# Performance work log

Hardware: AMD Instinct MI355X
Metric: run time of the kernel (lower is better)

Reference implementation:

```python
import jax, jax.numpy as jnp
import numpy as np

ALPHA = 0.2  # LeakyReLU negative slope
NEG_BIG = -9e15

def setup_inputs() -> dict:
    key = jax.random.key(0)
    k1, k2, k3, k4 = jax.random.split(key, 4)
    B, N, Fin, Fout = 32, 1024, 64, 64
    x = jax.random.normal(k1, (B, N, Fin), dtype=jnp.float32)
    adj = jax.random.randint(k2, (B, N, N), 0, 2, dtype=jnp.int32)
    W = jax.random.normal(k3, (Fin, Fout), dtype=jnp.float32) * (1.414 / np.sqrt(Fin))
    a = jax.random.normal(k4, (2 * Fout, 1), dtype=jnp.float32) * 0.1
    return {"x": x, "adj": adj, "W": W, "a": a}

def reference(x, adj, W, a):
    # x: [B,N,Fin], adj: [B,N,N], W: [Fin,Fout], a: [2*Fout,1]
    h = jnp.einsum('bnf,fo->bno', x, W)               # [B,N,Fout]
    Fout = W.shape[1]
    a1 = a[:Fout, 0]                                   # source half
    a2 = a[Fout:, 0]                                   # target half
    # e_ij = leakyrelu(a1.h_i + a2.h_j)  (equivalent to concat+matmul)
    f = h @ a1                                         # [B,N]
    g = h @ a2                                         # [B,N]
    e = jax.nn.leaky_relu(f[:, :, None] + g[:, None, :], ALPHA)  # [B,N,N]
    att = jnp.where(adj > 0, e, jnp.float32(NEG_BIG))
    att = jax.nn.softmax(att, axis=2)                  # dropout p=0, eval mode
    h_prime = jnp.einsum('bij,bjo->bio', att, h)       # [B,N,Fout]
    return jax.nn.elu(h_prime)                         # concat=True -> elu
```

## Files before the change

kernel.cpp:

```cpp
#include <hip/hip_runtime.h>
#include <hip/hip_bf16.h>
#include <hip/hip_fp16.h>

#define NN 1024
#define FD 64
#define BB 32

typedef __attribute__((ext_vector_type(4))) float    f32x4;
typedef __attribute__((ext_vector_type(8))) _Float16 f16x8;

static __device__ __forceinline__ unsigned short f2hu(float x) {
  _Float16 h = (_Float16)x;
  return __builtin_bit_cast(unsigned short, h);
}
static __device__ __forceinline__ f16x8 bch(int4 v) {
  return __builtin_bit_cast(f16x8, v);
}

__global__ __launch_bounds__(256) void gat_k1(
    const float* __restrict__ x, const float* __restrict__ W,
    const float* __restrict__ av, float* __restrict__ fv,
    float* __restrict__ gv, unsigned short* __restrict__ hF)
{
  __shared__ __align__(16) float Wl[FD * FD];
  __shared__ __align__(16) float xl[FD * 68];
  __shared__ __align__(16) unsigned short tl[FD * 64];
  __shared__ __align__(16) float al[2 * FD];

  const int tid = threadIdx.x;
  const int b   = blockIdx.x >> 4;
  const int n0  = (blockIdx.x & 15) << 6;

  if (tid < 32) ((f32x4*)al)[tid] = ((const f32x4*)av)[tid];
  {
    const int r  = tid >> 2;
    const int cb = (tid & 3) << 2;
    const f32x4* Wg = (const f32x4*)W;
    const f32x4* xg = (const f32x4*)(x + ((size_t)(b * NN + n0)) * FD);
#pragma unroll
    for (int k = 0; k < 4; ++k) {
      f32x4 wv = Wg[r * 16 + cb + k];
      f32x4 xv = xg[r * 16 + cb + k];
      *(f32x4*)(Wl + r * FD + ((cb + k) << 2)) = wv;
      *(f32x4*)(xl + r * 68 + ((cb + k) << 2)) = xv;
    }
  }
  __syncthreads();

  const int r  = tid >> 2;
  const int o0 = (tid & 3) << 4;
  float acc[16];
#pragma unroll
  for (int i = 0; i < 16; ++i) acc[i] = 0.f;

#pragma unroll 8
  for (int f = 0; f < FD; ++f) {
    float xv = xl[r * 68 + f];
    const f32x4* wr = (const f32x4*)(Wl + f * FD + o0);
#pragma unroll
    for (int c = 0; c < 4; ++c) {
      f32x4 wv = wr[c];
      acc[c * 4 + 0] += xv * wv.x;
      acc[c * 4 + 1] += xv * wv.y;
      acc[c * 4 + 2] += xv * wv.z;
      acc[c * 4 + 3] += xv * wv.w;
    }
  }

  float fp = 0.f, gp = 0.f;
#pragma unroll
  for (int i = 0; i < 16; ++i) {
    fp += acc[i] * al[o0 + i];
    gp += acc[i] * al[FD + o0 + i];
  }
  fp += __shfl_xor(fp, 1); fp += __shfl_xor(fp, 2);
  gp += __shfl_xor(gp, 1); gp += __shfl_xor(gp, 2);
  if ((tid & 3) == 0) {
    fv[b * NN + n0 + r] = fp;
    gv[b * NN + n0 + r] = gp;
  }

#pragma unroll
  for (int i = 0; i < 16; ++i) {
    int o = o0 + i;
    tl[o * 64 + ((((r >> 3) ^ (o & 7)) << 3) | (r & 7))] = f2hu(acc[i]);
  }
  __syncthreads();

  {
    const int jt = n0 >> 6;
#pragma unroll
    for (int hh = 0; hh < 2; ++hh) {
      int u = tid + (hh << 8);
      int frag = u >> 6, l = u & 63;
      int o = ((frag >> 1) << 4) + (l & 15);
      int c = ((frag & 1) << 2) + (l >> 4);
      int4 v = *(const int4*)(tl + o * 64 + ((c ^ (o & 7)) << 3));
      *(int4*)(hF + ((((size_t)(b * 16 + jt)) * 8 + frag) * 64 + l) * 8) = v;
    }
  }
}

__global__ __launch_bounds__(256) void gat_k2(
    const int* __restrict__ adj, const float* __restrict__ fv,
    const float* __restrict__ gv, const unsigned short* __restrict__ hF,
    float* __restrict__ out)
{
  __shared__ __align__(16) float gl[NN];
  __shared__ float red[4];

  const int tid  = threadIdx.x;
  const int b    = blockIdx.x >> 4;
  const int i0   = (blockIdx.x & 15) << 6;
  const int lane = tid & 63, w = tid >> 6;
  const int m16  = lane & 15, hi = lane >> 4;
  const int bN   = b * NN;

  f32x4 g4 = *(const f32x4*)(gv + bN + tid * 4);
  *(f32x4*)(gl + tid * 4) = g4;
  float gm = fmaxf(fmaxf(g4.x, g4.y), fmaxf(g4.z, g4.w));
  float fm = fv[bN + i0 + lane];
#pragma unroll
  for (int m = 1; m < 64; m <<= 1) {
    gm = fmaxf(gm, __shfl_xor(gm, m));
    fm = fmaxf(fm, __shfl_xor(fm, m));
  }
  if (lane == 0) red[w] = gm;
  const float fr = fv[bN + i0 + w * 16 + m16];
  __syncthreads();
  gm = fmaxf(fmaxf(red[0], red[1]), fmaxf(red[2], red[3]));
  const float sm = fm + gm;
  const float Cb = fmaxf(sm, 0.2f * sm);

  const int*  adjP = adj + ((size_t)(bN + i0 + w * 16 + m16)) * NN + hi * 8;
  const int4* hFb  = (const int4*)hF + (size_t)b * 8192 + lane;

  float dAcc = 0.f;
  f32x4 acc[4];
#pragma unroll
  for (int n = 0; n < 4; ++n) acc[n] = (f32x4){0.f, 0.f, 0.f, 0.f};

  int4 Aa0, Aa1, Aa2, Aa3, Ba0, Ba1, Ba2, Ba3;

#define LADJ(P, t) do { const int o_ = (t) << 6;        \
    P##0 = *(const int4*)(adjP + o_);                   \
    P##1 = *(const int4*)(adjP + o_ + 4);               \
    P##2 = *(const int4*)(adjP + o_ + 32);              \
    P##3 = *(const int4*)(adjP + o_ + 36); } while (0)

#define PCOMP(dst, ia, ib, ga, gb) do {                                    \
    float e0 = fr + ga.x, e1 = fr + ga.y, e2 = fr + ga.z, e3 = fr + ga.w;  \
    float e4 = fr + gb.x, e5 = fr + gb.y, e6 = fr + gb.z, e7 = fr + gb.w;  \
    e0 = fmaxf(e0, 0.2f * e0) - Cb; e1 = fmaxf(e1, 0.2f * e1) - Cb;        \
    e2 = fmaxf(e2, 0.2f * e2) - Cb; e3 = fmaxf(e3, 0.2f * e3) - Cb;        \
    e4 = fmaxf(e4, 0.2f * e4) - Cb; e5 = fmaxf(e5, 0.2f * e5) - Cb;        \
    e6 = fmaxf(e6, 0.2f * e6) - Cb; e7 = fmaxf(e7, 0.2f * e7) - Cb;        \
    float p0 = (ia.x > 0) ? __expf(e0) : 0.f;                              \
    float p1 = (ia.y > 0) ? __expf(e1) : 0.f;                              \
    float p2 = (ia.z > 0) ? __expf(e2) : 0.f;                              \
    float p3 = (ia.w > 0) ? __expf(e3) : 0.f;                              \
    float p4 = (ib.x > 0) ? __expf(e4) : 0.f;                              \
    float p5 = (ib.y > 0) ? __expf(e5) : 0.f;                              \
    float p6 = (ib.z > 0) ? __expf(e6) : 0.f;                              \
    float p7 = (ib.w > 0) ? __expf(e7) : 0.f;                              \
    dAcc += ((p0 + p1) + (p2 + p3)) + ((p4 + p5) + (p6 + p7));             \
    dst = (f16x8){(_Float16)p0, (_Float16)p1, (_Float16)p2, (_Float16)p3,  \
                  (_Float16)p4, (_Float16)p5, (_Float16)p6, (_Float16)p7}; \
  } while (0)

#define TILE(P, t) do {                                                    \
    const int jb_ = (t) << 6;                                              \
    const int4* hp_ = hFb + (size_t)(t) * 512;                             \
    int4 h0_ = hp_[0],   h1_ = hp_[64],  h2_ = hp_[128], h3_ = hp_[192];   \
    int4 h4_ = hp_[256], h5_ = hp_[320], h6_ = hp_[384], h7_ = hp_[448];   \
    f32x4 ga0_ = *(const f32x4*)(gl + jb_ + hi * 8);                       \
    f32x4 ga1_ = *(const f32x4*)(gl + jb_ + hi * 8 + 4);                   \
    f32x4 gb0_ = *(const f32x4*)(gl + jb_ + 32 + hi * 8);                  \
    f32x4 gb1_ = *(const f32x4*)(gl + jb_ + 32 + hi * 8 + 4);              \
    f16x8 pa_, pb_;                                                        \
    PCOMP(pa_, P##0, P##1, ga0_, ga1_);                                    \
    PCOMP(pb_, P##2, P##3, gb0_, gb1_);                                    \
    acc[0] = __builtin_amdgcn_mfma_f32_16x16x32_f16(pa_, bch(h0_), acc[0], 0, 0, 0); \
    acc[0] = __builtin_amdgcn_mfma_f32_16x16x32_f16(pb_, bch(h1_), acc[0], 0, 0, 0); \
    acc[1] = __builtin_amdgcn_mfma_f32_16x16x32_f16(pa_, bch(h2_), acc[1], 0, 0, 0); \
    acc[1] = __builtin_amdgcn_mfma_f32_16x16x32_f16(pb_, bch(h3_), acc[1], 0, 0, 0); \
    acc[2] = __builtin_amdgcn_mfma_f32_16x16x32_f16(pa_, bch(h4_), acc[2], 0, 0, 0); \
    acc[2] = __builtin_amdgcn_mfma_f32_16x16x32_f16(pb_, bch(h5_), acc[2], 0, 0, 0); \
    acc[3] = __builtin_amdgcn_mfma_f32_16x16x32_f16(pa_, bch(h6_), acc[3], 0, 0, 0); \
    acc[3] = __builtin_amdgcn_mfma_f32_16x16x32_f16(pb_, bch(h7_), acc[3], 0, 0, 0); \
  } while (0)

  LADJ(Aa, 0);
  for (int tt = 0; tt < 8; ++tt) {
    LADJ(Ba, 2 * tt + 1);
    TILE(Aa, 2 * tt);
    if (tt < 7) LADJ(Aa, 2 * tt + 2);
    TILE(Ba, 2 * tt + 1);
  }

  dAcc += __shfl_xor(dAcc, 16);
  dAcc += __shfl_xor(dAcc, 32);

  float* outB = out + ((size_t)(bN + i0 + w * 16)) * FD;
#pragma unroll
  for (int rr = 0; rr < 4; ++rr) {
    const int lr = hi * 4 + rr;
    float d   = __shfl(dAcc, lr);
    float inv = d > 0.f ? 1.f / d : 0.f;
#pragma unroll
    for (int n = 0; n < 4; ++n) {
      float v = acc[n][rr] * inv;
      v = v > 0.f ? v : (__expf(v) - 1.f);
      outB[(size_t)lr * FD + n * 16 + m16] = v;
    }
  }
#undef LADJ
#undef PCOMP
#undef TILE
}

extern "C" void kernel_launch(void* const* d_in, const int* in_sizes, int n_in,
                              void* d_out, int out_size, void* d_ws, size_t ws_size,
                              hipStream_t stream) {
  const float* x   = (const float*)d_in[0];
  const int*   adj = (const int*)d_in[1];
  const float* W   = (const float*)d_in[2];
  const float* a   = (const float*)d_in[3];
  float* out = (float*)d_out;

  unsigned short* hF = (unsigned short*)d_ws;
  float* fv = (float*)((char*)d_ws + (size_t)BB * FD * NN * 2);
  float* gv = fv + (size_t)BB * NN;

  gat_k1<<<dim3(BB * 16), dim3(256), 0, stream>>>(x, W, a, fv, gv, hF);
  gat_k2<<<dim3(BB * 16), dim3(256), 0, stream>>>(adj, fv, gv, hF, out);
}
```

Measured before the change: 44.30 us.

## Pack adjacency into bitmask in first kernel and consume bits in attention kernel

Merges the projection kernel with a new adjacency-packing pass: 4 of every 5 blocks read int32 adj rows and write a per-lane-ordered bitmask, so the attention kernel reads 1 bit per edge instead of 4 bytes. The attention loop is also rewritten to double-buffer the h fragment loads across tiles. The full adj array is still read once in the first kernel, so total traffic barely drops. The gain depends on that read running with better parallelism in the wider grid, and on the second kernel overlapping more compute with its now smaller loads.

```diff
diff --git a/kernel.cpp b/kernel.cpp
--- a/kernel.cpp
+++ b/kernel.cpp
@@ -17,93 +17,135 @@
   return __builtin_bit_cast(f16x8, v);
 }
 
-__global__ __launch_bounds__(256) void gat_k1(
+__global__ __launch_bounds__(256) void gat_k01(
     const float* __restrict__ x, const float* __restrict__ W,
-    const float* __restrict__ av, float* __restrict__ fv,
-    float* __restrict__ gv, unsigned short* __restrict__ hF)
+    const float* __restrict__ av, const int* __restrict__ adj,
+    float* __restrict__ fv, float* __restrict__ gv,
+    unsigned short* __restrict__ hF, unsigned* __restrict__ maskG)
 {
-  __shared__ __align__(16) float Wl[FD * FD];
-  __shared__ __align__(16) float xl[FD * 68];
-  __shared__ __align__(16) unsigned short tl[FD * 64];
-  __shared__ __align__(16) float al[2 * FD];
-
+  __shared__ __align__(16) char smem[43008];
   const int tid = threadIdx.x;
-  const int b   = blockIdx.x >> 4;
-  const int n0  = (blockIdx.x & 15) << 6;
-
-  if (tid < 32) ((f32x4*)al)[tid] = ((const f32x4*)av)[tid];
-  {
+  const int id  = blockIdx.x;
+
+  if (id % 5 == 0) {
+    const int kb = id / 5;
+    float*          Wl = (float*)smem;
+    float*          xl = (float*)(smem + 16384);
+    unsigned short* tl = (unsigned short*)(smem + 33792);
+    float*          al = (float*)(smem + 41984);
+
+    const int b  = kb >> 4;
+    const int n0 = (kb & 15) << 6;
+
+    if (tid < 32) ((f32x4*)al)[tid] = ((const f32x4*)av)[tid];
+    {
+      const int r  = tid >> 2;
+      const int cb = (tid & 3) << 2;
+      const f32x4* Wg = (const f32x4*)W;
+      const f32x4* xg = (const f32x4*)(x + ((size_t)(b * NN + n0)) * FD);
+#pragma unroll
+      for (int k = 0; k < 4; ++k) {
+        f32x4 wv = Wg[r * 16 + cb + k];
+        f32x4 xv = xg[r * 16 + cb + k];
+        *(f32x4*)(Wl + r * FD + ((cb + k) << 2)) = wv;
+        *(f32x4*)(xl + r * 68 + ((cb + k) << 2)) = xv;
+      }
+    }
+    __syncthreads();
+
     const int r  = tid >> 2;
-    const int cb = (tid & 3) << 2;
-    const f32x4* Wg = (const f32x4*)W;
-    const f32x4* xg = (const f32x4*)(x + ((size_t)(b * NN + n0)) * FD);
-#pragma unroll
-    for (int k = 0; k < 4; ++k) {
-      f32x4 wv = Wg[r * 16 + cb + k];
-      f32x4 xv = xg[r * 16 + cb + k];
-      *(f32x4*)(Wl + r * FD + ((cb + k) << 2)) = wv;
-      *(f32x4*)(xl + r * 68 + ((cb + k) << 2)) = xv;
-    }
-  }
-  __syncthreads();
-
-  const int r  = tid >> 2;
-  const int o0 = (tid & 3) << 4;
-  float acc[16];
-#pragma unroll
-  for (int i = 0; i < 16; ++i) acc[i] = 0.f;
+    const int o0 = (tid & 3) << 4;
+    float acc[16];
+#pragma unroll
+    for (int i = 0; i < 16; ++i) acc[i] = 0.f;
 
 #pragma unroll 8
-  for (int f = 0; f < FD; ++f) {
-    float xv = xl[r * 68 + f];
-    const f32x4* wr = (const f32x4*)(Wl + f * FD + o0);
-#pragma unroll
-    for (int c = 0; c < 4; ++c) {
-      f32x4 wv = wr[c];
-      acc[c * 4 + 0] += xv * wv.x;
-      acc[c * 4 + 1] += xv * wv.y;
-      acc[c * 4 + 2] += xv * wv.z;
-      acc[c * 4 + 3] += xv * wv.w;
-    }
-  }
-
-  float fp = 0.f, gp = 0.f;
-#pragma unroll
-  for (int i = 0; i < 16; ++i) {
-    fp += acc[i] * al[o0 + i];
-    gp += acc[i] * al[FD + o0 + i];
-  }
-  fp += __shfl_xor(fp, 1); fp += __shfl_xor(fp, 2);
-  gp += __shfl_xor(gp, 1); gp += __shfl_xor(gp, 2);
-  if ((tid & 3) == 0) {
-    fv[b * NN + n0 + r] = fp;
-    gv[b * NN + n0 + r] = gp;
-  }
-
-#pragma unroll
-  for (int i = 0; i < 16; ++i) {
-    int o = o0 + i;
-    tl[o * 64 + ((((r >> 3) ^ (o & 7)) << 3) | (r & 7))] = f2hu(acc[i]);
-  }
-  __syncthreads();
-
-  {
-    const int jt = n0 >> 6;
-#pragma unroll
-    for (int hh = 0; hh < 2; ++hh) {
-      int u = tid + (hh << 8);
-      int frag = u >> 6, l = u & 63;
-      int o = ((frag >> 1) << 4) + (l & 15);
-      int c = ((frag & 1) << 2) + (l >> 4);
-      int4 v = *(const int4*)(tl + o * 64 + ((c ^ (o & 7)) << 3));
-      *(int4*)(hF + ((((size_t)(b * 16 + jt)) * 8 + frag) * 64 + l) * 8) = v;
+    for (int f = 0; f < FD; ++f) {
+      float xv = xl[r * 68 + f];
+      const f32x4* wr = (const f32x4*)(Wl + f * FD + o0);
+#pragma unroll
+      for (int c = 0; c < 4; ++c) {
+        f32x4 wv = wr[c];
+        acc[c * 4 + 0] += xv * wv.x;
+        acc[c * 4 + 1] += xv * wv.y;
+        acc[c * 4 + 2] += xv * wv.z;
+        acc[c * 4 + 3] += xv * wv.w;
+      }
+    }
+
+    float fp = 0.f, gp = 0.f;
+#pragma unroll
+    for (int i = 0; i < 16; ++i) {
+      fp += acc[i] * al[o0 + i];
+      gp += acc[i] * al[FD + o0 + i];
+    }
+    fp += __shfl_xor(fp, 1); fp += __shfl_xor(fp, 2);
+    gp += __shfl_xor(gp, 1); gp += __shfl_xor(gp, 2);
+    if ((tid & 3) == 0) {
+      fv[b * NN + n0 + r] = fp;
+      gv[b * NN + n0 + r] = gp;
+    }
+
+#pragma unroll
+    for (int i = 0; i < 16; ++i) {
+      int o = o0 + i;
+      tl[o * 64 + ((((r >> 3) ^ (o & 7)) << 3) | (r & 7))] = f2hu(acc[i]);
+    }
+    __syncthreads();
+    {
+      const int jt = n0 >> 6;
+#pragma unroll
+      for (int hh = 0; hh < 2; ++hh) {
+        int u = tid + (hh << 8);
+        int frag = u >> 6, l = u & 63;
+        int o = ((frag >> 1) << 4) + (l & 15);
+        int c = ((frag & 1) << 2) + (l >> 4);
+        int4 v = *(const int4*)(tl + o * 64 + ((c ^ (o & 7)) << 3));
+        *(int4*)(hF + ((((size_t)(b * 16 + jt)) * 8 + frag) * 64 + l) * 8) = v;
+      }
+    }
+  } else {
+    const int c  = id - id / 5 - 1;
+    unsigned* mbuf = (unsigned*)smem;
+    const int b = c >> 6, G = c & 63;
+    const int w = tid >> 6, l = tid & 63;
+    const int rr = l >> 4, col16 = l & 15;
+    const int row = G * 16 + w * 4 + rr;
+    const int4* src = (const int4*)(adj + ((size_t)(b * NN + row)) * NN) + col16;
+
+    int4 v[16];
+#pragma unroll
+    for (int q = 0; q < 16; ++q) v[q] = src[q * 16];
+
+#pragma unroll
+    for (int q = 0; q < 16; ++q) {
+      int4 a = v[q];
+      unsigned nib = (unsigned)a.x | ((unsigned)a.y << 1) |
+                     ((unsigned)a.z << 2) | ((unsigned)a.w << 3);
+      unsigned nb  = nib | ((unsigned)__shfl_xor((int)nib, 1) << 4);
+      if (!(l & 1)) {
+        const int hi   = (l >> 1) & 3;
+        const int half = (l >> 3) & 1;
+        const int lam  = hi * 16 + w * 4 + rr;
+        const int p    = q >> 1;
+        const int bp   = (q & 1) * 2 + half;
+        ((char*)smem)[(lam + p * 64) * 4 + bp] = (char)(nb & 0xff);
+      }
+    }
+    __syncthreads();
+    {
+      const int lam = tid >> 2, p0 = (tid & 3) * 2;
+      unsigned w0 = mbuf[lam + p0 * 64];
+      unsigned w1 = mbuf[lam + p0 * 64 + 64];
+      uint2 o; o.x = w0; o.y = w1;
+      *(uint2*)(maskG + (((size_t)(b * 64 + G) * 64 + lam) * 8 + p0)) = o;
     }
   }
 }
 
 __global__ __launch_bounds__(256) void gat_k2(
-    const int* __restrict__ adj, const float* __restrict__ fv,
-    const float* __restrict__ gv, const unsigned short* __restrict__ hF,
+    const float* __restrict__ fv, const float* __restrict__ gv,
+    const unsigned short* __restrict__ hF, const unsigned* __restrict__ maskG,
     float* __restrict__ out)
 {
   __shared__ __align__(16) float gl[NN];
@@ -132,71 +174,70 @@
   const float sm = fm + gm;
   const float Cb = fmaxf(sm, 0.2f * sm);
 
-  const int*  adjP = adj + ((size_t)(bN + i0 + w * 16 + m16)) * NN + hi * 8;
-  const int4* hFb  = (const int4*)hF + (size_t)b * 8192 + lane;
+  const uint4* mp = (const uint4*)(maskG +
+      ((size_t)(b * 64 + (blockIdx.x & 15) * 4 + w) * 64 + lane) * 8);
+  const uint4 mA = mp[0], mB = mp[1];
+  const unsigned mq[8] = {mA.x, mA.y, mA.z, mA.w, mB.x, mB.y, mB.z, mB.w};
+
+  const int4* hFb = (const int4*)hF + (size_t)b * 8192 + lane;
 
   float dAcc = 0.f;
   f32x4 acc[4];
 #pragma unroll
   for (int n = 0; n < 4; ++n) acc[n] = (f32x4){0.f, 0.f, 0.f, 0.f};
 
-  int4 Aa0, Aa1, Aa2, Aa3, Ba0, Ba1, Ba2, Ba3;
-
-#define LADJ(P, t) do { const int o_ = (t) << 6;        \
-    P##0 = *(const int4*)(adjP + o_);                   \
-    P##1 = *(const int4*)(adjP + o_ + 4);               \
-    P##2 = *(const int4*)(adjP + o_ + 32);              \
-    P##3 = *(const int4*)(adjP + o_ + 36); } while (0)
-
-#define PCOMP(dst, ia, ib, ga, gb) do {                                    \
+#define PCOMP(dst, bits, ga, gb) do {                                      \
     float e0 = fr + ga.x, e1 = fr + ga.y, e2 = fr + ga.z, e3 = fr + ga.w;  \
     float e4 = fr + gb.x, e5 = fr + gb.y, e6 = fr + gb.z, e7 = fr + gb.w;  \
     e0 = fmaxf(e0, 0.2f * e0) - Cb; e1 = fmaxf(e1, 0.2f * e1) - Cb;        \
     e2 = fmaxf(e2, 0.2f * e2) - Cb; e3 = fmaxf(e3, 0.2f * e3) - Cb;        \
     e4 = fmaxf(e4, 0.2f * e4) - Cb; e5 = fmaxf(e5, 0.2f * e5) - Cb;        \
     e6 = fmaxf(e6, 0.2f * e6) - Cb; e7 = fmaxf(e7, 0.2f * e7) - Cb;        \
-    float p0 = (ia.x > 0) ? __expf(e0) : 0.f;                              \
-    float p1 = (ia.y > 0) ? __expf(e1) : 0.f;                              \
-    float p2 = (ia.z > 0) ? __expf(e2) : 0.f;                              \
-    float p3 = (ia.w > 0) ? __expf(e3) : 0.f;                              \
-    float p4 = (ib.x > 0) ? __expf(e4) : 0.f;                              \
-    float p5 = (ib.y > 0) ? __expf(e5) : 0.f;                              \
-    float p6 = (ib.z > 0) ? __expf(e6) : 0.f;                              \
-    float p7 = (ib.w > 0) ? __expf(e7) : 0.f;                              \
+    float p0 = (bits & 1u)   ? __expf(e0) : 0.f;                           \
+    float p1 = (bits & 2u)   ? __expf(e1) : 0.f;                           \
+    float p2 = (bits & 4u)   ? __expf(e2) : 0.f;                           \
+    float p3 = (bits & 8u)   ? __expf(e3) : 0.f;                           \
+    float p4 = (bits & 16u)  ? __expf(e4) : 0.f;                           \
+    float p5 = (bits & 32u)  ? __expf(e5) : 0.f;                           \
+    float p6 = (bits & 64u)  ? __expf(e6) : 0.f;                           \
+    float p7 = (bits & 128u) ? __expf(e7) : 0.f;                           \
     dAcc += ((p0 + p1) + (p2 + p3)) + ((p4 + p5) + (p6 + p7));             \
     dst = (f16x8){(_Float16)p0, (_Float16)p1, (_Float16)p2, (_Float16)p3,  \
                   (_Float16)p4, (_Float16)p5, (_Float16)p6, (_Float16)p7}; \
   } while (0)
 
-#define TILE(P, t) do {                                                    \
-    const int jb_ = (t) << 6;                                              \
-    const int4* hp_ = hFb + (size_t)(t) * 512;                             \
-    int4 h0_ = hp_[0],   h1_ = hp_[64],  h2_ = hp_[128], h3_ = hp_[192];   \
-    int4 h4_ = hp_[256], h5_ = hp_[320], h6_ = hp_[384], h7_ = hp_[448];   \
-    f32x4 ga0_ = *(const f32x4*)(gl + jb_ + hi * 8);                       \
-    f32x4 ga1_ = *(const f32x4*)(gl + jb_ + hi * 8 + 4);                   \
-    f32x4 gb0_ = *(const f32x4*)(gl + jb_ + 32 + hi * 8);                  \
-    f32x4 gb1_ = *(const f32x4*)(gl + jb_ + 32 + hi * 8 + 4);              \
-    f16x8 pa_, pb_;                                                        \
-    PCOMP(pa_, P##0, P##1, ga0_, ga1_);                                    \
-    PCOMP(pb_, P##2, P##3, gb0_, gb1_);                                    \
-    acc[0] = __builtin_amdgcn_mfma_f32_16x16x32_f16(pa_, bch(h0_), acc[0], 0, 0, 0); \
-    acc[0] = __builtin_amdgcn_mfma_f32_16x16x32_f16(pb_, bch(h1_), acc[0], 0, 0, 0); \
-    acc[1] = __builtin_amdgcn_mfma_f32_16x16x32_f16(pa_, bch(h2_), acc[1], 0, 0, 0); \
-    acc[1] = __builtin_amdgcn_mfma_f32_16x16x32_f16(pb_, bch(h3_), acc[1], 0, 0, 0); \
-    acc[2] = __builtin_amdgcn_mfma_f32_16x16x32_f16(pa_, bch(h4_), acc[2], 0, 0, 0); \
-    acc[2] = __builtin_amdgcn_mfma_f32_16x16x32_f16(pb_, bch(h5_), acc[2], 0, 0, 0); \
-    acc[3] = __builtin_amdgcn_mfma_f32_16x16x32_f16(pa_, bch(h6_), acc[3], 0, 0, 0); \
-    acc[3] = __builtin_amdgcn_mfma_f32_16x16x32_f16(pb_, bch(h7_), acc[3], 0, 0, 0); \
-  } while (0)
-
-  LADJ(Aa, 0);
-  for (int tt = 0; tt < 8; ++tt) {
-    LADJ(Ba, 2 * tt + 1);
-    TILE(Aa, 2 * tt);
-    if (tt < 7) LADJ(Aa, 2 * tt + 2);
-    TILE(Ba, 2 * tt + 1);
-  }
+  int4 h[2][8];
+#pragma unroll
+  for (int k = 0; k < 8; ++k) h[0][k] = hFb[k * 64];
+
+#pragma unroll
+  for (int t = 0; t < 16; ++t) {
+    const int cur = t & 1, nxt = cur ^ 1;
+    if (t < 15) {
+      const int4* hp = hFb + (size_t)(t + 1) * 512;
+#pragma unroll
+      for (int k = 0; k < 8; ++k) h[nxt][k] = hp[k * 64];
+    }
+    const unsigned mwrd = mq[t >> 1] >> ((t & 1) * 16);
+    const unsigned ab = mwrd & 0xffu, bb = (mwrd >> 8) & 0xffu;
+    const int jb = t * 64;
+    f32x4 ga0 = *(const f32x4*)(gl + jb + hi * 8);
+    f32x4 ga1 = *(const f32x4*)(gl + jb + hi * 8 + 4);
+    f32x4 gb0 = *(const f32x4*)(gl + jb + 32 + hi * 8);
+    f32x4 gb1 = *(const f32x4*)(gl + jb + 32 + hi * 8 + 4);
+    f16x8 pa, pb;
+    PCOMP(pa, ab, ga0, ga1);
+    PCOMP(pb, bb, gb0, gb1);
+    acc[0] = __builtin_amdgcn_mfma_f32_16x16x32_f16(pa, bch(h[cur][0]), acc[0], 0, 0, 0);
+    acc[0] = __builtin_amdgcn_mfma_f32_16x16x32_f16(pb, bch(h[cur][1]), acc[0], 0, 0, 0);
+    acc[1] = __builtin_amdgcn_mfma_f32_16x16x32_f16(pa, bch(h[cur][2]), acc[1], 0, 0, 0);
+    acc[1] = __builtin_amdgcn_mfma_f32_16x16x32_f16(pb, bch(h[cur][3]), acc[1], 0, 0, 0);
+    acc[2] = __builtin_amdgcn_mfma_f32_16x16x32_f16(pa, bch(h[cur][4]), acc[2], 0, 0, 0);
+    acc[2] = __builtin_amdgcn_mfma_f32_16x16x32_f16(pb, bch(h[cur][5]), acc[2], 0, 0, 0);
+    acc[3] = __builtin_amdgcn_mfma_f32_16x16x32_f16(pa, bch(h[cur][6]), acc[3], 0, 0, 0);
+    acc[3] = __builtin_amdgcn_mfma_f32_16x16x32_f16(pb, bch(h[cur][7]), acc[3], 0, 0, 0);
+  }
+#undef PCOMP
 
   dAcc += __shfl_xor(dAcc, 16);
   dAcc += __shfl_xor(dAcc, 32);
@@ -214,9 +255,6 @@
       outB[(size_t)lr * FD + n * 16 + m16] = v;
     }
   }
-#undef LADJ
-#undef PCOMP
-#undef TILE
 }
 
 extern "C" void kernel_launch(void* const* d_in, const int* in_sizes, int n_in,
@@ -228,10 +266,11 @@
   const float* a   = (const float*)d_in[3];
   float* out = (float*)d_out;
 
-  unsigned short* hF = (unsigned short*)d_ws;
+  unsigned short* hT = (unsigned short*)d_ws;
   float* fv = (float*)((char*)d_ws + (size_t)BB * FD * NN * 2);
   float* gv = fv + (size_t)BB * NN;
-
-  gat_k1<<<dim3(BB * 16), dim3(256), 0, stream>>>(x, W, a, fv, gv, hF);
-  gat_k2<<<dim3(BB * 16), dim3(256), 0, stream>>>(adj, fv, gv, hF, out);
-}
+  unsigned* maskG = (unsigned*)(gv + (size_t)BB * NN);
+
+  gat_k01<<<dim3(2560), dim3(256), 0, stream>>>(x, W, a, adj, fv, gv, hT, maskG);
+  gat_k2<<<dim3(BB * 16), dim3(256), 0, stream>>>(fv, gv, hT, maskG, out);
+}
```

Result: slower. 70.02 us (+58.0%).

## Split attention reduction across waves along j with LDS cross-wave combine

Applied to the files above, without the earlier changes.

Each block of gat_k2 now handles 16 rows instead of 64. Its four waves each cover a quarter of the 1024 neighbours (split-K), and the partial accumulators and denominators are combined through shared memory. The grid grows fourfold, which raises parallelism and shortens each wave's serial chain of 16 tiles to 4. Adjacency loads and output stores become nontemporal so the streaming adj matrix does not pollute the cache. The cost is extra LDS traffic, a block barrier, and each block reloading g and the h fragments for fewer rows.

```diff
diff --git a/kernel.cpp b/kernel.cpp
--- a/kernel.cpp
+++ b/kernel.cpp
@@ -8,6 +8,7 @@
 
 typedef __attribute__((ext_vector_type(4))) float    f32x4;
 typedef __attribute__((ext_vector_type(8))) _Float16 f16x8;
+typedef __attribute__((ext_vector_type(4))) int      i32x4;
 
 static __device__ __forceinline__ unsigned short f2hu(float x) {
   _Float16 h = (_Float16)x;
@@ -86,7 +87,6 @@
     tl[o * 64 + ((((r >> 3) ^ (o & 7)) << 3) | (r & 7))] = f2hu(acc[i]);
   }
   __syncthreads();
-
   {
     const int jt = n0 >> 6;
 #pragma unroll
@@ -108,10 +108,12 @@
 {
   __shared__ __align__(16) float gl[NN];
   __shared__ float red[4];
+  __shared__ __align__(16) float accb[4096];
+  __shared__ float dpart[4][16];
 
   const int tid  = threadIdx.x;
-  const int b    = blockIdx.x >> 4;
-  const int i0   = (blockIdx.x & 15) << 6;
+  const int b    = blockIdx.x >> 6;
+  const int i0   = (blockIdx.x & 63) << 4;
   const int lane = tid & 63, w = tid >> 6;
   const int m16  = lane & 15, hi = lane >> 4;
   const int bN   = b * NN;
@@ -119,34 +121,34 @@
   f32x4 g4 = *(const f32x4*)(gv + bN + tid * 4);
   *(f32x4*)(gl + tid * 4) = g4;
   float gm = fmaxf(fmaxf(g4.x, g4.y), fmaxf(g4.z, g4.w));
-  float fm = fv[bN + i0 + lane];
-#pragma unroll
-  for (int m = 1; m < 64; m <<= 1) {
-    gm = fmaxf(gm, __shfl_xor(gm, m));
-    fm = fmaxf(fm, __shfl_xor(fm, m));
-  }
+#pragma unroll
+  for (int m = 1; m < 64; m <<= 1) gm = fmaxf(gm, __shfl_xor(gm, m));
   if (lane == 0) red[w] = gm;
-  const float fr = fv[bN + i0 + w * 16 + m16];
+  const float fr = fv[bN + i0 + m16];
+  float fm = fr;
+#pragma unroll
+  for (int m = 1; m < 16; m <<= 1) fm = fmaxf(fm, __shfl_xor(fm, m));
   __syncthreads();
   gm = fmaxf(fmaxf(red[0], red[1]), fmaxf(red[2], red[3]));
   const float sm = fm + gm;
   const float Cb = fmaxf(sm, 0.2f * sm);
 
-  const int*  adjP = adj + ((size_t)(bN + i0 + w * 16 + m16)) * NN + hi * 8;
+  const int*  adjP = adj + ((size_t)(bN + i0 + m16)) * NN + w * 256 + hi * 8;
   const int4* hFb  = (const int4*)hF + (size_t)b * 8192 + lane;
+  const int   w4   = w * 4;
 
   float dAcc = 0.f;
   f32x4 acc[4];
 #pragma unroll
   for (int n = 0; n < 4; ++n) acc[n] = (f32x4){0.f, 0.f, 0.f, 0.f};
 
-  int4 Aa0, Aa1, Aa2, Aa3, Ba0, Ba1, Ba2, Ba3;
-
-#define LADJ(P, t) do { const int o_ = (t) << 6;        \
-    P##0 = *(const int4*)(adjP + o_);                   \
-    P##1 = *(const int4*)(adjP + o_ + 4);               \
-    P##2 = *(const int4*)(adjP + o_ + 32);              \
-    P##3 = *(const int4*)(adjP + o_ + 36); } while (0)
+  i32x4 Aa0, Aa1, Aa2, Aa3, Ba0, Ba1, Ba2, Ba3;
+
+#define LADJ(P, t) do { const int* p_ = adjP + ((t) << 6);       \
+    P##0 = __builtin_nontemporal_load((const i32x4*)(p_));       \
+    P##1 = __builtin_nontemporal_load((const i32x4*)(p_ + 4));   \
+    P##2 = __builtin_nontemporal_load((const i32x4*)(p_ + 32));  \
+    P##3 = __builtin_nontemporal_load((const i32x4*)(p_ + 36)); } while (0)
 
 #define PCOMP(dst, ia, ib, ga, gb) do {                                    \
     float e0 = fr + ga.x, e1 = fr + ga.y, e2 = fr + ga.z, e3 = fr + ga.w;  \
@@ -168,18 +170,19 @@
                   (_Float16)p4, (_Float16)p5, (_Float16)p6, (_Float16)p7}; \
   } while (0)
 
-#define TILE(P, t) do {                                                    \
-    const int jb_ = (t) << 6;                                              \
-    const int4* hp_ = hFb + (size_t)(t) * 512;                             \
+#define TILE(t, P) do {                                                    \
+    const int jt_ = w4 + (t);                                              \
+    const int4* hp_ = hFb + (size_t)jt_ * 512;                             \
     int4 h0_ = hp_[0],   h1_ = hp_[64],  h2_ = hp_[128], h3_ = hp_[192];   \
     int4 h4_ = hp_[256], h5_ = hp_[320], h6_ = hp_[384], h7_ = hp_[448];   \
-    f32x4 ga0_ = *(const f32x4*)(gl + jb_ + hi * 8);                       \
-    f32x4 ga1_ = *(const f32x4*)(gl + jb_ + hi * 8 + 4);                   \
-    f32x4 gb0_ = *(const f32x4*)(gl + jb_ + 32 + hi * 8);                  \
-    f32x4 gb1_ = *(const f32x4*)(gl + jb_ + 32 + hi * 8 + 4);              \
+    const float* gp_ = gl + jt_ * 64 + hi * 8;                             \
+    f32x4 ga0_ = *(const f32x4*)(gp_);                                     \
+    f32x4 ga1_ = *(const f32x4*)(gp_ + 4);                                 \
+    f32x4 gc0_ = *(const f32x4*)(gp_ + 32);                                \
+    f32x4 gc1_ = *(const f32x4*)(gp_ + 36);                                \
     f16x8 pa_, pb_;                                                        \
     PCOMP(pa_, P##0, P##1, ga0_, ga1_);                                    \
-    PCOMP(pb_, P##2, P##3, gb0_, gb1_);                                    \
+    PCOMP(pb_, P##2, P##3, gc0_, gc1_);                                    \
     acc[0] = __builtin_amdgcn_mfma_f32_16x16x32_f16(pa_, bch(h0_), acc[0], 0, 0, 0); \
     acc[0] = __builtin_amdgcn_mfma_f32_16x16x32_f16(pb_, bch(h1_), acc[0], 0, 0, 0); \
     acc[1] = __builtin_amdgcn_mfma_f32_16x16x32_f16(pa_, bch(h2_), acc[1], 0, 0, 0); \
@@ -190,33 +193,40 @@
     acc[3] = __builtin_amdgcn_mfma_f32_16x16x32_f16(pb_, bch(h7_), acc[3], 0, 0, 0); \
   } while (0)
 
-  LADJ(Aa, 0);
-  for (int tt = 0; tt < 8; ++tt) {
-    LADJ(Ba, 2 * tt + 1);
-    TILE(Aa, 2 * tt);
-    if (tt < 7) LADJ(Aa, 2 * tt + 2);
-    TILE(Ba, 2 * tt + 1);
-  }
-
-  dAcc += __shfl_xor(dAcc, 16);
-  dAcc += __shfl_xor(dAcc, 32);
-
-  float* outB = out + ((size_t)(bN + i0 + w * 16)) * FD;
-#pragma unroll
-  for (int rr = 0; rr < 4; ++rr) {
-    const int lr = hi * 4 + rr;
-    float d   = __shfl(dAcc, lr);
-    float inv = d > 0.f ? 1.f / d : 0.f;
-#pragma unroll
-    for (int n = 0; n < 4; ++n) {
-      float v = acc[n][rr] * inv;
-      v = v > 0.f ? v : (__expf(v) - 1.f);
-      outB[(size_t)lr * FD + n * 16 + m16] = v;
-    }
-  }
+  LADJ(Aa, 0); LADJ(Ba, 1);
+  TILE(0, Aa); LADJ(Aa, 2);
+  TILE(1, Ba); LADJ(Ba, 3);
+  TILE(2, Aa);
+  TILE(3, Ba);
 #undef LADJ
 #undef PCOMP
 #undef TILE
+
+  dAcc += __shfl_xor(dAcc, 16);
+  dAcc += __shfl_xor(dAcc, 32);
+  if (lane < 16) dpart[w][lane] = dAcc;
+
+#pragma unroll
+  for (int n = 0; n < 4; ++n)
+#pragma unroll
+    for (int rr = 0; rr < 4; ++rr)
+      accb[((w * 4 + n) * 4 + rr) * 64 + lane] = acc[n][rr];
+  __syncthreads();
+
+  float* outB = out + ((size_t)(bN + i0)) * FD + w * 16 + m16;
+#pragma unroll
+  for (int rr = 0; rr < 4; ++rr) {
+    const int lr = hi * 4 + rr;
+    float d = dpart[0][lr] + dpart[1][lr] + dpart[2][lr] + dpart[3][lr];
+    float inv = d > 0.f ? 1.f / d : 0.f;
+    float v = (accb[((0 * 4 + w) * 4 + rr) * 64 + lane] +
+               accb[((1 * 4 + w) * 4 + rr) * 64 + lane]) +
+              (accb[((2 * 4 + w) * 4 + rr) * 64 + lane] +
+               accb[((3 * 4 + w) * 4 + rr) * 64 + lane]);
+    v *= inv;
+    v = v > 0.f ? v : (__expf(v) - 1.f);
+    __builtin_nontemporal_store(v, outB + (size_t)lr * FD);
+  }
 }
 
 extern "C" void kernel_launch(void* const* d_in, const int* in_sizes, int n_in,
@@ -233,5 +243,5 @@
   float* gv = fv + (size_t)BB * NN;
 
   gat_k1<<<dim3(BB * 16), dim3(256), 0, stream>>>(x, W, a, fv, gv, hF);
-  gat_k2<<<dim3(BB * 16), dim3(256), 0, stream>>>(adj, fv, gv, hF, out);
-}
+  gat_k2<<<dim3(BB * 64), dim3(256), 0, stream>>>(adj, fv, gv, hF, out);
+}
```

After: 60.02 us. 1.35x slower.

## Double-buffer adjacency and h-fragment loads in attention kernel with nontemporal access

Applied to the files above, without the earlier changes.

The main loop of gat_k2 is fully unrolled into explicit steps with two register buffers for both the adjacency tile and the fp16 h fragments. Loads for tile t+2 are issued during the compute of tile t, so global load latency is hidden behind the exp and MFMA work. Adjacency loads and output stores now use nontemporal hints, and launch bounds request two blocks per SM. The extra prefetched registers raise register pressure, and the occupancy hint could cap registers or cause spills.

```diff
diff --git a/kernel.cpp b/kernel.cpp
--- a/kernel.cpp
+++ b/kernel.cpp
@@ -8,6 +8,7 @@
 
 typedef __attribute__((ext_vector_type(4))) float    f32x4;
 typedef __attribute__((ext_vector_type(8))) _Float16 f16x8;
+typedef __attribute__((ext_vector_type(4))) int      i32x4;
 
 static __device__ __forceinline__ unsigned short f2hu(float x) {
   _Float16 h = (_Float16)x;
@@ -86,7 +87,6 @@
     tl[o * 64 + ((((r >> 3) ^ (o & 7)) << 3) | (r & 7))] = f2hu(acc[i]);
   }
   __syncthreads();
-
   {
     const int jt = n0 >> 6;
 #pragma unroll
@@ -101,7 +101,7 @@
   }
 }
 
-__global__ __launch_bounds__(256) void gat_k2(
+__global__ __launch_bounds__(256, 2) void gat_k2(
     const int* __restrict__ adj, const float* __restrict__ fv,
     const float* __restrict__ gv, const unsigned short* __restrict__ hF,
     float* __restrict__ out)
@@ -140,13 +140,20 @@
 #pragma unroll
   for (int n = 0; n < 4; ++n) acc[n] = (f32x4){0.f, 0.f, 0.f, 0.f};
 
-  int4 Aa0, Aa1, Aa2, Aa3, Ba0, Ba1, Ba2, Ba3;
-
-#define LADJ(P, t) do { const int o_ = (t) << 6;        \
-    P##0 = *(const int4*)(adjP + o_);                   \
-    P##1 = *(const int4*)(adjP + o_ + 4);               \
-    P##2 = *(const int4*)(adjP + o_ + 32);              \
-    P##3 = *(const int4*)(adjP + o_ + 36); } while (0)
+  i32x4 A0_0, A0_1, A0_2, A0_3, A1_0, A1_1, A1_2, A1_3;
+  int4  H0_0, H0_1, H0_2, H0_3, H0_4, H0_5, H0_6, H0_7;
+  int4  H1_0, H1_1, H1_2, H1_3, H1_4, H1_5, H1_6, H1_7;
+
+#define LADJ(P, t) do { const int* p_ = adjP + ((t) << 6);       \
+    P##_0 = __builtin_nontemporal_load((const i32x4*)(p_));      \
+    P##_1 = __builtin_nontemporal_load((const i32x4*)(p_ + 4));  \
+    P##_2 = __builtin_nontemporal_load((const i32x4*)(p_ + 32)); \
+    P##_3 = __builtin_nontemporal_load((const i32x4*)(p_ + 36)); } while (0)
+
+#define LHF(P, t) do { const int4* hp_ = hFb + (size_t)(t) * 512; \
+    P##_0 = hp_[0];   P##_1 = hp_[64];  P##_2 = hp_[128];         \
+    P##_3 = hp_[192]; P##_4 = hp_[256]; P##_5 = hp_[320];         \
+    P##_6 = hp_[384]; P##_7 = hp_[448]; } while (0)
 
 #define PCOMP(dst, ia, ib, ga, gb) do {                                    \
     float e0 = fr + ga.x, e1 = fr + ga.y, e2 = fr + ga.z, e3 = fr + ga.w;  \
@@ -168,35 +175,43 @@
                   (_Float16)p4, (_Float16)p5, (_Float16)p6, (_Float16)p7}; \
   } while (0)
 
-#define TILE(P, t) do {                                                    \
-    const int jb_ = (t) << 6;                                              \
-    const int4* hp_ = hFb + (size_t)(t) * 512;                             \
-    int4 h0_ = hp_[0],   h1_ = hp_[64],  h2_ = hp_[128], h3_ = hp_[192];   \
-    int4 h4_ = hp_[256], h5_ = hp_[320], h6_ = hp_[384], h7_ = hp_[448];   \
-    f32x4 ga0_ = *(const f32x4*)(gl + jb_ + hi * 8);                       \
-    f32x4 ga1_ = *(const f32x4*)(gl + jb_ + hi * 8 + 4);                   \
-    f32x4 gb0_ = *(const f32x4*)(gl + jb_ + 32 + hi * 8);                  \
-    f32x4 gb1_ = *(const f32x4*)(gl + jb_ + 32 + hi * 8 + 4);              \
+#define STEP(t, AP, HP, PRE) do {                                          \
+    const float* gp_ = gl + (t) * 64 + hi * 8;                             \
+    f32x4 ga0_ = *(const f32x4*)(gp_);                                     \
+    f32x4 ga1_ = *(const f32x4*)(gp_ + 4);                                 \
+    f32x4 gb0_ = *(const f32x4*)(gp_ + 32);                                \
+    f32x4 gb1_ = *(const f32x4*)(gp_ + 36);                                \
     f16x8 pa_, pb_;                                                        \
-    PCOMP(pa_, P##0, P##1, ga0_, ga1_);                                    \
-    PCOMP(pb_, P##2, P##3, gb0_, gb1_);                                    \
-    acc[0] = __builtin_amdgcn_mfma_f32_16x16x32_f16(pa_, bch(h0_), acc[0], 0, 0, 0); \
-    acc[0] = __builtin_amdgcn_mfma_f32_16x16x32_f16(pb_, bch(h1_), acc[0], 0, 0, 0); \
-    acc[1] = __builtin_amdgcn_mfma_f32_16x16x32_f16(pa_, bch(h2_), acc[1], 0, 0, 0); \
-    acc[1] = __builtin_amdgcn_mfma_f32_16x16x32_f16(pb_, bch(h3_), acc[1], 0, 0, 0); \
-    acc[2] = __builtin_amdgcn_mfma_f32_16x16x32_f16(pa_, bch(h4_), acc[2], 0, 0, 0); \
-    acc[2] = __builtin_amdgcn_mfma_f32_16x16x32_f16(pb_, bch(h5_), acc[2], 0, 0, 0); \
-    acc[3] = __builtin_amdgcn_mfma_f32_16x16x32_f16(pa_, bch(h6_), acc[3], 0, 0, 0); \
-    acc[3] = __builtin_amdgcn_mfma_f32_16x16x32_f16(pb_, bch(h7_), acc[3], 0, 0, 0); \
+    PCOMP(pa_, AP##_0, AP##_1, ga0_, ga1_);                                \
+    PCOMP(pb_, AP##_2, AP##_3, gb0_, gb1_);                                \
+    if (PRE) LADJ(AP, (t) + 2);                                            \
+    acc[0] = __builtin_amdgcn_mfma_f32_16x16x32_f16(pa_, bch(HP##_0), acc[0], 0, 0, 0); \
+    acc[0] = __builtin_amdgcn_mfma_f32_16x16x32_f16(pb_, bch(HP##_1), acc[0], 0, 0, 0); \
+    acc[1] = __builtin_amdgcn_mfma_f32_16x16x32_f16(pa_, bch(HP##_2), acc[1], 0, 0, 0); \
+    acc[1] = __builtin_amdgcn_mfma_f32_16x16x32_f16(pb_, bch(HP##_3), acc[1], 0, 0, 0); \
+    acc[2] = __builtin_amdgcn_mfma_f32_16x16x32_f16(pa_, bch(HP##_4), acc[2], 0, 0, 0); \
+    acc[2] = __builtin_amdgcn_mfma_f32_16x16x32_f16(pb_, bch(HP##_5), acc[2], 0, 0, 0); \
+    acc[3] = __builtin_amdgcn_mfma_f32_16x16x32_f16(pa_, bch(HP##_6), acc[3], 0, 0, 0); \
+    acc[3] = __builtin_amdgcn_mfma_f32_16x16x32_f16(pb_, bch(HP##_7), acc[3], 0, 0, 0); \
+    if (PRE) LHF(HP, (t) + 2);                                             \
   } while (0)
 
-  LADJ(Aa, 0);
-  for (int tt = 0; tt < 8; ++tt) {
-    LADJ(Ba, 2 * tt + 1);
-    TILE(Aa, 2 * tt);
-    if (tt < 7) LADJ(Aa, 2 * tt + 2);
-    TILE(Ba, 2 * tt + 1);
-  }
+  LADJ(A0, 0); LHF(H0, 0);
+  LADJ(A1, 1); LHF(H1, 1);
+
+  STEP(0,  A0, H0, 1); STEP(1,  A1, H1, 1);
+  STEP(2,  A0, H0, 1); STEP(3,  A1, H1, 1);
+  STEP(4,  A0, H0, 1); STEP(5,  A1, H1, 1);
+  STEP(6,  A0, H0, 1); STEP(7,  A1, H1, 1);
+  STEP(8,  A0, H0, 1); STEP(9,  A1, H1, 1);
+  STEP(10, A0, H0, 1); STEP(11, A1, H1, 1);
+  STEP(12, A0, H0, 1); STEP(13, A1, H1, 1);
+  STEP(14, A0, H0, 0); STEP(15, A1, H1, 0);
+
+#undef LADJ
+#undef LHF
+#undef PCOMP
+#undef STEP
 
   dAcc += __shfl_xor(dAcc, 16);
   dAcc += __shfl_xor(dAcc, 32);
@@ -211,12 +226,9 @@
     for (int n = 0; n < 4; ++n) {
       float v = acc[n][rr] * inv;
       v = v > 0.f ? v : (__expf(v) - 1.f);
-      outB[(size_t)lr * FD + n * 16 + m16] = v;
-    }
-  }
-#undef LADJ
-#undef PCOMP
-#undef TILE
+      __builtin_nontemporal_store(v, outB + (size_t)lr * FD + n * 16 + m16);
+    }
+  }
 }
 
 extern "C" void kernel_launch(void* const* d_in, const int* in_sizes, int n_in,
```

Measured after the change: 59.15 us. 1.34x slower.
